# Optimization experiments

Hardware: AMD Instinct MI355X
Metric: run time of the kernel (lower is better)

The kernel has to match this reference:

```python
import jax, jax.numpy as jnp
import numpy as np

O, T = 100000, 400000
DIN = HID = DOUT = 128


def setup_inputs() -> dict:
    key = jax.random.key(0)
    ks = jax.random.split(key, 12)
    s = lambda fan_in: 1.0 / np.sqrt(fan_in)
    inp = {
        "obj_vecs": jax.random.normal(ks[0], (O, DIN), jnp.float32),
        "pred_vecs": jax.random.normal(ks[1], (T, DIN), jnp.float32),
        "edges": jax.random.randint(ks[2], (T, 2), 0, O, jnp.int64 if jax.config.read("jax_enable_x64") else jnp.int32),
        # net1: Linear(3*Din -> H), ReLU, Linear(H -> 2H + Dout)
        "W1a": jax.random.uniform(ks[3], (3 * DIN, HID), jnp.float32, -s(3 * DIN), s(3 * DIN)),
        "b1a": jax.random.uniform(ks[4], (HID,), jnp.float32, -s(3 * DIN), s(3 * DIN)),
        "W1b": jax.random.uniform(ks[5], (HID, 2 * HID + DOUT), jnp.float32, -s(HID), s(HID)),
        "b1b": jax.random.uniform(ks[6], (2 * HID + DOUT,), jnp.float32, -s(HID), s(HID)),
        # net2: Linear(H -> H), ReLU, Linear(H -> Dout)
        "W2a": jax.random.uniform(ks[7], (HID, HID), jnp.float32, -s(HID), s(HID)),
        "b2a": jax.random.uniform(ks[8], (HID,), jnp.float32, -s(HID), s(HID)),
        "W2b": jax.random.uniform(ks[9], (HID, DOUT), jnp.float32, -s(HID), s(HID)),
        "b2b": jax.random.uniform(ks[10], (DOUT,), jnp.float32, -s(HID), s(HID)),
    }
    return inp


def reference(obj_vecs, pred_vecs, edges, W1a, b1a, W1b, b1b, W2a, b2a, W2b, b2b):
    s_idx = edges[:, 0]
    o_idx = edges[:, 1]
    # 1. Triple formation: [h_s || r || h_o]  -> (T, 3*Din)
    t = jnp.concatenate([obj_vecs[s_idx], pred_vecs, obj_vecs[o_idx]], axis=1)
    # 2. net1 MLP
    h = jax.nn.relu(t @ W1a + b1a)
    new_t = h @ W1b + b1b  # (T, 2H + Dout)
    new_s = new_t[:, :HID]
    new_p = new_t[:, HID:HID + DOUT]
    new_o = new_t[:, HID + DOUT:]
    # 3. Scatter-add messages to nodes
    pooled = jax.ops.segment_sum(new_s, s_idx, num_segments=O)
    pooled = pooled + jax.ops.segment_sum(new_o, o_idx, num_segments=O)
    # 4. Average pooling by neighbor count (clamped to >= 1)
    ones = jnp.ones((T,), pooled.dtype)
    counts = jax.ops.segment_sum(ones, s_idx, num_segments=O)
    counts = counts + jax.ops.segment_sum(ones, o_idx, num_segments=O)
    pooled = pooled / jnp.maximum(counts, 1.0)[:, None]
    # 5. net2 node update
    new_obj = jax.nn.relu(pooled @ W2a + b2a) @ W2b + b2b
    return new_obj, new_p
```

## Files before the change

### kernel.cpp

```cpp
#include <hip/hip_runtime.h>
#include <hip/hip_bf16.h>
#include <stdint.h>

#define O_N 100000
#define T_N 400000
#define NCH1 1563
#define NCH3 391
#define NCHW 25000

typedef __attribute__((ext_vector_type(8))) short short8;
typedef __attribute__((ext_vector_type(4))) unsigned short us4;
typedef __attribute__((ext_vector_type(4))) float f32x4;
typedef __attribute__((ext_vector_type(16))) float f32x16;
typedef unsigned short ushort_t;

__device__ __forceinline__ unsigned short f2bf(float x) {
    union { float f; unsigned u; } v; v.f = x;
    unsigned u = v.u;
    unsigned rounded = u + 0x7FFF + ((u >> 16) & 1);
    return (unsigned short)(rounded >> 16);
}

__device__ __forceinline__ short8 pack8(f32x4 a, f32x4 b) {
    short8 t;
    t[0] = (short)f2bf(a[0]); t[1] = (short)f2bf(a[1]);
    t[2] = (short)f2bf(a[2]); t[3] = (short)f2bf(a[3]);
    t[4] = (short)f2bf(b[0]); t[5] = (short)f2bf(b[1]);
    t[6] = (short)f2bf(b[2]); t[7] = (short)f2bf(b[3]);
    return t;
}

__global__ void pack_b32(const float* __restrict__ W, ushort_t* __restrict__ out,
                         int Ksteps, int NT, int ldw, int col0) {
    int idx = blockIdx.x * 256 + threadIdx.x;
    int total = Ksteps * NT * 512;
    if (idx >= total) return;
    int j = idx & 7;
    int lane = (idx >> 3) & 63;
    int t2 = idx >> 9;
    int nt = t2 % NT;
    int ks = t2 / NT;
    int k = ks * 16 + ((lane >> 5) << 3) + j;
    int n = col0 + (nt << 5) + (lane & 31);
    out[idx] = f2bf(W[(size_t)k * ldw + n]);
}

__global__ void pack_b(const float* __restrict__ W, unsigned short* __restrict__ out,
                       int K, int Ntiles, int ldw, int col0) {
    int idx = blockIdx.x * 256 + threadIdx.x;
    int total = K * Ntiles * 16;
    if (idx >= total) return;
    int j = idx & 7;
    int lane = (idx >> 3) & 63;
    int t2 = idx >> 9;
    int ntile = t2 % Ntiles;
    int kstep = t2 / Ntiles;
    int k = kstep * 32 + ((lane >> 4) << 3) + j;
    int n = (ntile << 4) + (lane & 15);
    out[idx] = f2bf(W[(size_t)k * ldw + col0 + n]);
}

__global__ void counts_k(const int* __restrict__ edges, float* __restrict__ counts) {
    int idx = blockIdx.x * 256 + threadIdx.x;
    if (idx >= T_N) return;
    int2 e = ((const int2*)edges)[idx];
    atomicAdd(&counts[e.x], 1.0f);
    atomicAdd(&counts[e.y], 1.0f);
}

__global__ __launch_bounds__(1024, 4) void gemm1_k(
    const float* __restrict__ obj_vecs, const float* __restrict__ pred_vecs,
    const int* __restrict__ edges,
    const ushort_t* __restrict__ W1a_p, const float* __restrict__ b1a,
    ushort_t* __restrict__ hbuf)
{
    __shared__ __align__(16) ushort_t Wl[49152];
    __shared__ __align__(16) ushort_t hx[16][1088];
    const int tid = threadIdx.x;
    const int l = tid & 63;
    const int w = tid >> 6;
    const int r16 = l & 15;
    const int kq = l >> 4;

    {
        const short8* s = reinterpret_cast<const short8*>(W1a_p);
        short8* d = reinterpret_cast<short8*>(Wl);
        #pragma unroll
        for (int i = 0; i < 6; ++i) d[i * 1024 + tid] = s[i * 1024 + tid];
    }
    __syncthreads();

    float bias[8];
    #pragma unroll
    for (int nt = 0; nt < 8; ++nt) bias[nt] = b1a[nt * 16 + r16];

    ushort_t* hw = hx[w];
    const int2* e2 = (const int2*)edges;
    const int stride = gridDim.x * 16;

    for (int ch = blockIdx.x * 16 + w; ch < NCHW; ch += stride) {
        int tri = ch * 16 + r16;
        int2 e = e2[tri];
        const float* ps = obj_vecs  + (size_t)e.x * 128;
        const float* pp = pred_vecs + (size_t)tri * 128;
        const float* po = obj_vecs  + (size_t)e.y * 128;

        f32x4 acc[8];
        #pragma unroll
        for (int nt = 0; nt < 8; ++nt) acc[nt] = (f32x4){0.f, 0.f, 0.f, 0.f};

        {
            short8 af[4];
            #pragma unroll
            for (int ks = 0; ks < 4; ++ks) {
                f32x4 v0 = *reinterpret_cast<const f32x4*>(ps + ks * 32 + kq * 8);
                f32x4 v1 = *reinterpret_cast<const f32x4*>(ps + ks * 32 + kq * 8 + 4);
                af[ks] = pack8(v0, v1);
            }
            #pragma unroll
            for (int ks = 0; ks < 4; ++ks)
                #pragma unroll
                for (int nt = 0; nt < 8; ++nt) {
                    short8 b = *reinterpret_cast<const short8*>(&Wl[((ks * 8 + nt) * 64 + l) * 8]);
                    acc[nt] = __builtin_amdgcn_mfma_f32_16x16x32_bf16(af[ks], b, acc[nt], 0, 0, 0);
                }
        }
        {
            short8 af[4];
            #pragma unroll
            for (int ks = 0; ks < 4; ++ks) {
                f32x4 v0 = *reinterpret_cast<const f32x4*>(pp + ks * 32 + kq * 8);
                f32x4 v1 = *reinterpret_cast<const f32x4*>(pp + ks * 32 + kq * 8 + 4);
                af[ks] = pack8(v0, v1);
            }
            #pragma unroll
            for (int ks = 0; ks < 4; ++ks)
                #pragma unroll
                for (int nt = 0; nt < 8; ++nt) {
                    short8 b = *reinterpret_cast<const short8*>(&Wl[(((ks + 4) * 8 + nt) * 64 + l) * 8]);
                    acc[nt] = __builtin_amdgcn_mfma_f32_16x16x32_bf16(af[ks], b, acc[nt], 0, 0, 0);
                }
        }
        {
            short8 af[4];
            #pragma unroll
            for (int ks = 0; ks < 4; ++ks) {
                f32x4 v0 = *reinterpret_cast<const f32x4*>(po + ks * 32 + kq * 8);
                f32x4 v1 = *reinterpret_cast<const f32x4*>(po + ks * 32 + kq * 8 + 4);
                af[ks] = pack8(v0, v1);
            }
            #pragma unroll
            for (int ks = 0; ks < 4; ++ks)
                #pragma unroll
                for (int nt = 0; nt < 8; ++nt) {
                    short8 b = *reinterpret_cast<const short8*>(&Wl[(((ks + 8) * 8 + nt) * 64 + l) * 8]);
                    acc[nt] = __builtin_amdgcn_mfma_f32_16x16x32_bf16(af[ks], b, acc[nt], 0, 0, 0);
                }
        }

        #pragma unroll
        for (int p = 0; p < 2; ++p) {
            #pragma unroll
            for (int nt2 = 0; nt2 < 4; ++nt2) {
                int nt = p * 4 + nt2;
                #pragma unroll
                for (int j = 0; j < 4; ++j) {
                    int row = kq * 4 + j;
                    float hv = fmaxf(acc[nt][j] + bias[nt], 0.0f);
                    hw[row * 68 + nt2 * 16 + r16] = f2bf(hv);
                }
            }
            asm volatile("s_waitcnt lgkmcnt(0)" ::: "memory");
            #pragma unroll
            for (int it = 0; it < 2; ++it) {
                short8 hv = *reinterpret_cast<const short8*>(&hw[(l >> 2) * 68 + (l & 3) * 16 + it * 8]);
                *reinterpret_cast<short8*>(
                    &hbuf[(size_t)(ch * 16 + (l >> 2)) * 128 + p * 64 + (l & 3) * 16 + it * 8]) = hv;
            }
            asm volatile("s_waitcnt lgkmcnt(0)" ::: "memory");
        }
    }
}

__global__ __launch_bounds__(512, 2) void gemm2_k(
    const ushort_t* __restrict__ hbuf, const int* __restrict__ edges,
    const ushort_t* __restrict__ W1b_p, const float* __restrict__ b1b,
    ushort_t* __restrict__ pooled_bf, float* __restrict__ new_p)
{
    __shared__ __align__(16) ushort_t Wl[49152];
    const int tid = threadIdx.x;
    const int l = tid & 63;
    const int w = tid >> 6;
    const int q = l >> 5;
    const int r32 = l & 31;

    {
        const short8* s = reinterpret_cast<const short8*>(W1b_p);
        short8* d = reinterpret_cast<short8*>(Wl);
        #pragma unroll
        for (int i = 0; i < 12; ++i) d[i * 512 + tid] = s[i * 512 + tid];
    }
    __syncthreads();

    float bias[12];
    #pragma unroll
    for (int nt = 0; nt < 12; ++nt) bias[nt] = b1b[(nt << 5) + r32];

    for (int c = blockIdx.x; c < NCH1; c += gridDim.x) {
        int trow = c * 256 + w * 32 + r32;
        int tr = trow < T_N ? trow : T_N - 1;

        short8 af[8];
        #pragma unroll
        for (int ks = 0; ks < 8; ++ks)
            af[ks] = *reinterpret_cast<const short8*>(&hbuf[(size_t)tr * 128 + (ks << 4) + (q << 3)]);

        #pragma unroll
        for (int g = 0; g < 3; ++g) {
            f32x16 acc[4] = {};
            #pragma unroll
            for (int ks = 0; ks < 8; ++ks) {
                #pragma unroll
                for (int nt2 = 0; nt2 < 4; ++nt2) {
                    short8 bf = *reinterpret_cast<const short8*>(&Wl[((ks * 12 + (g << 2) + nt2) * 64 + l) * 8]);
                    acc[nt2] = __builtin_amdgcn_mfma_f32_32x32x16_bf16(af[ks], bf, acc[nt2], 0, 0, 0);
                }
            }
            if (g == 1) {
                #pragma unroll
                for (int nt2 = 0; nt2 < 4; ++nt2) {
                    #pragma unroll
                    for (int r = 0; r < 16; ++r) {
                        int rl = (r & 3) + ((r >> 2) << 3) + (q << 2);
                        int trow2 = c * 256 + w * 32 + rl;
                        if (trow2 < T_N)
                            new_p[(size_t)trow2 * 128 + (nt2 << 5) + r32] = acc[nt2][r] + bias[4 + nt2];
                    }
                }
            } else {
                #pragma unroll
                for (int r = 0; r < 16; ++r) {
                    int rl = (r & 3) + ((r >> 2) << 3) + (q << 2);
                    int trow2 = c * 256 + w * 32 + rl;
                    bool v2 = trow2 < T_N;
                    int t2 = v2 ? trow2 : T_N - 1;
                    int2 e2 = ((const int2*)edges)[t2];
                    int seg = (g == 0) ? e2.x : e2.y;
                    ushort_t* pb = pooled_bf + (size_t)seg * 128;
                    #pragma unroll
                    for (int nt2 = 0; nt2 < 4; ++nt2) {
                        float val = acc[nt2][r] + bias[(g << 2) + nt2];
                        float other = __shfl_xor(val, 1, 64);
                        if (v2 && !(r32 & 1)) {
                            unsigned dat = (unsigned)f2bf(val) | ((unsigned)f2bf(other) << 16);
                            uint64_t addr = (uint64_t)(uintptr_t)(pb + (nt2 << 5) + r32);
                            asm volatile("global_atomic_pk_add_bf16 %0, %1, off"
                                         :: "v"(addr), "v"(dat) : "memory");
                        }
                    }
                }
            }
        }
    }
}

__global__ __launch_bounds__(512, 2) void objects_k32(
    const ushort_t* __restrict__ pooled_bf, const float* __restrict__ counts,
    const ushort_t* __restrict__ W2a_p, const float* __restrict__ b2a,
    const ushort_t* __restrict__ W2b_p, const float* __restrict__ b2b,
    float* __restrict__ outp)
{
    __shared__ __align__(16) ushort_t Wa[16384];
    __shared__ __align__(16) ushort_t Wb[16384];
    __shared__ __align__(16) ushort_t hx[8][4096];
    const int tid = threadIdx.x;
    const int l = tid & 63;
    const int w = tid >> 6;
    const int q = l >> 5;
    const int r32 = l & 31;

    {
        const short8* sa = reinterpret_cast<const short8*>(W2a_p);
        const short8* sb = reinterpret_cast<const short8*>(W2b_p);
        short8* da = reinterpret_cast<short8*>(Wa);
        short8* db = reinterpret_cast<short8*>(Wb);
        #pragma unroll
        for (int i = 0; i < 4; ++i) { da[i * 512 + tid] = sa[i * 512 + tid]; db[i * 512 + tid] = sb[i * 512 + tid]; }
    }
    __syncthreads();

    float ba[4], bb[4];
    #pragma unroll
    for (int nt = 0; nt < 4; ++nt) { ba[nt] = b2a[(nt << 5) + r32]; bb[nt] = b2b[(nt << 5) + r32]; }

    for (int c = blockIdx.x; c < NCH3; c += gridDim.x) {
        int row = c * 256 + w * 32 + r32;
        int rr = row < O_N ? row : O_N - 1;
        float inv = 1.0f / fmaxf(counts[rr], 1.0f);

        short8 af[8];
        #pragma unroll
        for (int ks = 0; ks < 8; ++ks) {
            short8 raw = *reinterpret_cast<const short8*>(&pooled_bf[(size_t)rr * 128 + (ks << 4) + (q << 3)]);
            short8 a;
            #pragma unroll
            for (int j = 0; j < 8; ++j) {
                union { float f; unsigned u; } t;
                t.u = ((unsigned)(unsigned short)raw[j]) << 16;
                a[j] = (short)f2bf(t.f * inv);
            }
            af[ks] = a;
        }

        f32x16 acc[4] = {};
        #pragma unroll
        for (int ks = 0; ks < 8; ++ks) {
            #pragma unroll
            for (int nt = 0; nt < 4; ++nt) {
                short8 bf = *reinterpret_cast<const short8*>(&Wa[(((ks << 2) + nt) * 64 + l) * 8]);
                acc[nt] = __builtin_amdgcn_mfma_f32_32x32x16_bf16(af[ks], bf, acc[nt], 0, 0, 0);
            }
        }

        char* hxw = (char*)&hx[w][0];
        #pragma unroll
        for (int nt = 0; nt < 4; ++nt) {
            #pragma unroll
            for (int r = 0; r < 16; ++r) {
                int rl = (r & 3) + ((r >> 2) << 3) + (q << 2);
                float hv = fmaxf(acc[nt][r] + ba[nt], 0.0f);
                int off = rl * 256 + (((nt << 5) + r32) << 1);
                off ^= (rl & 15) << 4;
                *(ushort_t*)(hxw + off) = f2bf(hv);
            }
        }
        __syncthreads();

        short8 af2[8];
        #pragma unroll
        for (int ks = 0; ks < 8; ++ks) {
            int off = r32 * 256 + (ks << 5) + (q << 4);
            off ^= (r32 & 15) << 4;
            af2[ks] = *reinterpret_cast<const short8*>(hxw + off);
        }

        f32x16 acc2[4] = {};
        #pragma unroll
        for (int ks = 0; ks < 8; ++ks) {
            #pragma unroll
            for (int nt = 0; nt < 4; ++nt) {
                short8 bf = *reinterpret_cast<const short8*>(&Wb[(((ks << 2) + nt) * 64 + l) * 8]);
                acc2[nt] = __builtin_amdgcn_mfma_f32_32x32x16_bf16(af2[ks], bf, acc2[nt], 0, 0, 0);
            }
        }

        #pragma unroll
        for (int nt = 0; nt < 4; ++nt) {
            #pragma unroll
            for (int r = 0; r < 16; ++r) {
                int rl = (r & 3) + ((r >> 2) << 3) + (q << 2);
                int row2 = c * 256 + w * 32 + rl;
                if (row2 < O_N) outp[(size_t)row2 * 128 + (nt << 5) + r32] = acc2[nt][r] + bb[nt];
            }
        }
        __syncthreads();
    }
}

__device__ __forceinline__ void stage_w(const unsigned short* __restrict__ src,
                                        unsigned short* __restrict__ dst, int tid) {
    const short8* s = reinterpret_cast<const short8*>(src);
    short8* d = reinterpret_cast<short8*>(dst);
    d[tid] = s[tid];
    d[tid + 256] = s[tid + 256];
}

__global__ __launch_bounds__(256, 2) void triples_kernel(
    const float* __restrict__ obj_vecs, const float* __restrict__ pred_vecs,
    const int* __restrict__ edges,
    const unsigned short* __restrict__ W1a_p, const float* __restrict__ b1a,
    const unsigned short* __restrict__ W1b_p, const float* __restrict__ b1b,
    float* __restrict__ pooled, float* __restrict__ new_p, float* __restrict__ counts)
{
    __shared__ __align__(16) unsigned short Apack[24576];
    __shared__ __align__(16) unsigned short Wbuf[2][4096];
    __shared__ int sseg[64], oseg[64];
    const int tid = threadIdx.x;
    const int lane = tid & 63;
    const int w = tid >> 6;
    const int t0 = blockIdx.x * 64;
    if (tid < 64) {
        int s = edges[2 * (t0 + tid)];
        int o = edges[2 * (t0 + tid) + 1];
        sseg[tid] = s; oseg[tid] = o;
        atomicAdd(&counts[s], 1.0f);
        atomicAdd(&counts[o], 1.0f);
    }
    __syncthreads();
    for (int it = 0; it < 24; ++it) {
        int idx = it * 256 + tid;
        int r = idx / 96;
        int c = (idx % 96) * 4;
        const float* srcp;
        if (c < 128)      srcp = obj_vecs  + (size_t)sseg[r] * 128 + c;
        else if (c < 256) srcp = pred_vecs + (size_t)(t0 + r) * 128 + (c - 128);
        else              srcp = obj_vecs  + (size_t)oseg[r] * 128 + (c - 256);
        f32x4 v = *reinterpret_cast<const f32x4*>(srcp);
        int off = (((r >> 4) * 12 + (c >> 5)) << 9)
                + (((r & 15) | (((c & 31) >> 3) << 4)) << 3) + (c & 7);
        Apack[off + 0] = f2bf(v[0]); Apack[off + 1] = f2bf(v[1]);
        Apack[off + 2] = f2bf(v[2]); Apack[off + 3] = f2bf(v[3]);
    }
    stage_w(W1a_p, Wbuf[0], tid);
    __syncthreads();
    f32x4 acc[8];
    #pragma unroll
    for (int n = 0; n < 8; ++n) acc[n] = (f32x4){0.f, 0.f, 0.f, 0.f};
    for (int kk = 0; kk < 12; ++kk) {
        if (kk < 11) stage_w(W1a_p + (kk + 1) * 4096, Wbuf[(kk + 1) & 1], tid);
        short8 a = *reinterpret_cast<const short8*>(&Apack[((w * 12 + kk) << 9) + (lane << 3)]);
        const unsigned short* wb = Wbuf[kk & 1];
        #pragma unroll
        for (int n = 0; n < 8; ++n) {
            short8 b = *reinterpret_cast<const short8*>(&wb[((n << 6) + lane) << 3]);
            acc[n] = __builtin_amdgcn_mfma_f32_16x16x32_bf16(a, b, acc[n], 0, 0, 0);
        }
        __syncthreads();
    }
    #pragma unroll
    for (int n = 0; n < 8; ++n) {
        int col = (n << 4) + (lane & 15);
        float bias = b1a[col];
        int base = ((w * 4 + (col >> 5)) << 9) + (col & 7);
        int chi = ((col & 31) >> 3) << 4;
        #pragma unroll
        for (int jj = 0; jj < 4; ++jj) {
            int rloc = ((lane >> 4) << 2) + jj;
            float hv = acc[n][jj] + bias;
            hv = hv > 0.f ? hv : 0.f;
            Apack[base + ((rloc | chi) << 3)] = f2bf(hv);
        }
    }
    for (int g = 0; g < 3; ++g) {
        const unsigned short* Wsrc = W1b_p + g * 16384;
        stage_w(Wsrc, Wbuf[0], tid);
        __syncthreads();
        f32x4 acc2[8];
        #pragma unroll
        for (int n = 0; n < 8; ++n) acc2[n] = (f32x4){0.f, 0.f, 0.f, 0.f};
        for (int kk = 0; kk < 4; ++kk) {
            if (kk < 3) stage_w(Wsrc + (kk + 1) * 4096, Wbuf[(kk + 1) & 1], tid);
            short8 a = *reinterpret_cast<const short8*>(&Apack[((w * 4 + kk) << 9) + (lane << 3)]);
            const unsigned short* wb = Wbuf[kk & 1];
            #pragma unroll
            for (int n = 0; n < 8; ++n) {
                short8 b = *reinterpret_cast<const short8*>(&wb[((n << 6) + lane) << 3]);
                acc2[n] = __builtin_amdgcn_mfma_f32_16x16x32_bf16(a, b, acc2[n], 0, 0, 0);
            }
            __syncthreads();
        }
        #pragma unroll
        for (int n = 0; n < 8; ++n) {
            int col = (n << 4) + (lane & 15);
            float bias = b1b[g * 128 + col];
            #pragma unroll
            for (int jj = 0; jj < 4; ++jj) {
                int rloc = (w << 4) + ((lane >> 4) << 2) + jj;
                float val = acc2[n][jj] + bias;
                if (g == 1) {
                    new_p[(size_t)(t0 + rloc) * 128 + col] = val;
                } else {
                    int seg = (g == 0) ? sseg[rloc] : oseg[rloc];
                    atomicAdd(&pooled[(size_t)seg * 128 + col], val);
                }
            }
        }
    }
}

__global__ __launch_bounds__(256, 2) void objects_kernel(
    const float* __restrict__ counts,
    const unsigned short* __restrict__ W2a_p, const float* __restrict__ b2a,
    const unsigned short* __restrict__ W2b_p, const float* __restrict__ b2b,
    float* __restrict__ inout)
{
    __shared__ __align__(16) unsigned short Apack[8192];
    __shared__ __align__(16) unsigned short Hpack[8192];
    __shared__ __align__(16) unsigned short Wbuf[2][4096];
    const int tid = threadIdx.x;
    const int lane = tid & 63;
    const int w = tid >> 6;
    const int r0 = blockIdx.x * 64;
    for (int it = 0; it < 8; ++it) {
        int idx = it * 256 + tid;
        int r = idx >> 5;
        int c = (idx & 31) << 2;
        int row = r0 + r;
        float vals[4] = {0.f, 0.f, 0.f, 0.f};
        if (row < O_N) {
            f32x4 v = *reinterpret_cast<const f32x4*>(&inout[(size_t)row * 128 + c]);
            float inv = 1.0f / fmaxf(counts[row], 1.0f);
            vals[0] = v[0] * inv; vals[1] = v[1] * inv;
            vals[2] = v[2] * inv; vals[3] = v[3] * inv;
        }
        int off = (((r >> 4) * 4 + (c >> 5)) << 9)
                + (((r & 15) | (((c & 31) >> 3) << 4)) << 3) + (c & 7);
        Apack[off + 0] = f2bf(vals[0]); Apack[off + 1] = f2bf(vals[1]);
        Apack[off + 2] = f2bf(vals[2]); Apack[off + 3] = f2bf(vals[3]);
    }
    stage_w(W2a_p, Wbuf[0], tid);
    __syncthreads();
    f32x4 acc[8];
    #pragma unroll
    for (int n = 0; n < 8; ++n) acc[n] = (f32x4){0.f, 0.f, 0.f, 0.f};
    for (int kk = 0; kk < 4; ++kk) {
        if (kk < 3) stage_w(W2a_p + (kk + 1) * 4096, Wbuf[(kk + 1) & 1], tid);
        short8 a = *reinterpret_cast<const short8*>(&Apack[((w * 4 + kk) << 9) + (lane << 3)]);
        const unsigned short* wb = Wbuf[kk & 1];
        #pragma unroll
        for (int n = 0; n < 8; ++n) {
            short8 b = *reinterpret_cast<const short8*>(&wb[((n << 6) + lane) << 3]);
            acc[n] = __builtin_amdgcn_mfma_f32_16x16x32_bf16(a, b, acc[n], 0, 0, 0);
        }
        __syncthreads();
    }
    #pragma unroll
    for (int n = 0; n < 8; ++n) {
        int col = (n << 4) + (lane & 15);
        float bias = b2a[col];
        int base = ((w * 4 + (col >> 5)) << 9) + (col & 7);
        int chi = ((col & 31) >> 3) << 4;
        #pragma unroll
        for (int jj = 0; jj < 4; ++jj) {
            int rloc = ((lane >> 4) << 2) + jj;
            float hv = acc[n][jj] + bias;
            hv = hv > 0.f ? hv : 0.f;
            Hpack[base + ((rloc | chi) << 3)] = f2bf(hv);
        }
    }
    stage_w(W2b_p, Wbuf[0], tid);
    __syncthreads();
    f32x4 acc2[8];
    #pragma unroll
    for (int n = 0; n < 8; ++n) acc2[n] = (f32x4){0.f, 0.f, 0.f, 0.f};
    for (int kk = 0; kk < 4; ++kk) {
        if (kk < 3) stage_w(W2b_p + (kk + 1) * 4096, Wbuf[(kk + 1) & 1], tid);
        short8 a = *reinterpret_cast<const short8*>(&Hpack[((w * 4 + kk) << 9) + (lane << 3)]);
        const unsigned short* wb = Wbuf[kk & 1];
        #pragma unroll
        for (int n = 0; n < 8; ++n) {
            short8 b = *reinterpret_cast<const short8*>(&wb[((n << 6) + lane) << 3]);
            acc2[n] = __builtin_amdgcn_mfma_f32_16x16x32_bf16(a, b, acc2[n], 0, 0, 0);
        }
        __syncthreads();
    }
    #pragma unroll
    for (int n = 0; n < 8; ++n) {
        int col = (n << 4) + (lane & 15);
        float bias = b2b[col];
        #pragma unroll
        for (int jj = 0; jj < 4; ++jj) {
            int rloc = (w << 4) + ((lane >> 4) << 2) + jj;
            int row = r0 + rloc;
            if (row < O_N) inout[(size_t)row * 128 + col] = acc2[n][jj] + bias;
        }
    }
}

extern "C" void kernel_launch(void* const* d_in, const int* in_sizes, int n_in,
                              void* d_out, int out_size, void* d_ws, size_t ws_size,
                              hipStream_t stream)
{
    const float* obj   = (const float*)d_in[0];
    const float* pred  = (const float*)d_in[1];
    const int*   edges = (const int*)d_in[2];
    const float* W1a = (const float*)d_in[3];
    const float* b1a = (const float*)d_in[4];
    const float* W1b = (const float*)d_in[5];
    const float* b1b = (const float*)d_in[6];
    const float* W2a = (const float*)d_in[7];
    const float* b2a = (const float*)d_in[8];
    const float* W2b = (const float*)d_in[9];
    const float* b2b = (const float*)d_in[10];

    float* out    = (float*)d_out;
    float* new_p  = out + (size_t)O_N * 128;

    uintptr_t wsbase = (uintptr_t)d_ws;
    float* counts = (float*)wsbase;
    uintptr_t p = (wsbase + (size_t)O_N * 4 + 255) & ~(uintptr_t)255;
    ushort_t* pooled_bf = (ushort_t*)p;  p += (size_t)O_N * 128 * 2;
    ushort_t* W1a_p = (ushort_t*)p;  p += (size_t)49152 * 2;
    ushort_t* W1b_p = (ushort_t*)p;  p += (size_t)49152 * 2;
    ushort_t* W2a_p = (ushort_t*)p;  p += (size_t)16384 * 2;
    ushort_t* W2b_p = (ushort_t*)p;  p += (size_t)16384 * 2;
    ushort_t* hbuf  = (ushort_t*)p;  p += (size_t)T_N * 128 * 2;
    size_t need = p - wsbase;

    hipMemsetAsync(counts, 0, (size_t)O_N * sizeof(float), stream);

    if (ws_size >= need) {
        hipMemsetAsync(pooled_bf, 0, (size_t)O_N * 128 * 2, stream);

        pack_b<<<192, 256, 0, stream>>>(W1a, W1a_p, 384, 8, 128, 0);
        pack_b32<<<192, 256, 0, stream>>>(W1b, W1b_p, 8, 12, 384, 0);
        pack_b32<<<64, 256, 0, stream>>>(W2a, W2a_p, 8, 4, 128, 0);
        pack_b32<<<64, 256, 0, stream>>>(W2b, W2b_p, 8, 4, 128, 0);
        counts_k<<<(T_N + 255) / 256, 256, 0, stream>>>(edges, counts);

        gemm1_k<<<256, 1024, 0, stream>>>(obj, pred, edges, W1a_p, b1a, hbuf);
        gemm2_k<<<256, 512, 0, stream>>>(hbuf, edges, W1b_p, b1b, pooled_bf, new_p);
        objects_k32<<<391, 512, 0, stream>>>(pooled_bf, counts, W2a_p, b2a, W2b_p, b2b, out);
    } else {
        float* pooled = out;
        hipMemsetAsync(pooled, 0, (size_t)O_N * 128 * sizeof(float), stream);

        pack_b<<<192, 256, 0, stream>>>(W1a, W1a_p, 384, 8, 128, 0);
        pack_b<<<64, 256, 0, stream>>>(W1b, W1b_p,         128, 8, 384, 0);
        pack_b<<<64, 256, 0, stream>>>(W1b, W1b_p + 16384, 128, 8, 384, 128);
        pack_b<<<64, 256, 0, stream>>>(W1b, W1b_p + 32768, 128, 8, 384, 256);
        pack_b<<<64, 256, 0, stream>>>(W2a, W2a_p, 128, 8, 128, 0);
        pack_b<<<64, 256, 0, stream>>>(W2b, W2b_p, 128, 8, 128, 0);

        triples_kernel<<<T_N / 64, 256, 0, stream>>>(obj, pred, edges,
                                                     W1a_p, b1a, W1b_p, b1b,
                                                     pooled, new_p, counts);
        objects_kernel<<<(O_N + 63) / 64, 256, 0, stream>>>(counts, W2a_p, b2a, W2b_p, b2b, out);
    }
}
```

Measured before the change: 460.9 us.

## Scatter hidden activations before W1b and apply subject/object projections per node

Uses the linearity of the second net1 layer. The per-triple hidden vector h is scatter-added into per-node subject and object sums (Hs/Ho), and the W1b subject and object column blocks are applied once per node afterwards. Bias is added back scaled by the separate subject and object counts. This cuts gemm2 from three 128-column output groups per triple to only the new_p group, and moves mean normalisation into a new pooled_k node-level GEMM. The cost is an extra kernel and buffers aliased into the output region, while bf16 atomic accumulation now applies to h instead of to the outputs.

```diff
diff --git a/kernel.cpp b/kernel.cpp
--- a/kernel.cpp
+++ b/kernel.cpp
@@ -60,12 +60,27 @@
     out[idx] = f2bf(W[(size_t)k * ldw + col0 + n]);
 }
 
-__global__ void counts_k(const int* __restrict__ edges, float* __restrict__ counts) {
+__global__ void pack_bso(const float* __restrict__ W1b, ushort_t* __restrict__ out) {
+    int idx = blockIdx.x * 256 + threadIdx.x;
+    if (idx >= 32768) return;
+    int j = idx & 7;
+    int lane = (idx >> 3) & 63;
+    int t2 = idx >> 9;
+    int nt = t2 & 3;
+    int ks = t2 >> 2;
+    int k = ks * 16 + ((lane >> 5) << 3) + j;
+    int n = (nt << 5) + (lane & 31);
+    float v = (k < 128) ? W1b[(size_t)k * 384 + n] : W1b[(size_t)(k - 128) * 384 + 256 + n];
+    out[idx] = f2bf(v);
+}
+
+__global__ void counts_k(const int* __restrict__ edges,
+                         float* __restrict__ cs, float* __restrict__ co) {
     int idx = blockIdx.x * 256 + threadIdx.x;
     if (idx >= T_N) return;
     int2 e = ((const int2*)edges)[idx];
-    atomicAdd(&counts[e.x], 1.0f);
-    atomicAdd(&counts[e.y], 1.0f);
+    atomicAdd(&cs[e.x], 1.0f);
+    atomicAdd(&co[e.y], 1.0f);
 }
 
 __global__ __launch_bounds__(1024, 4) void gemm1_k(
@@ -182,90 +197,151 @@
     }
 }
 
-__global__ __launch_bounds__(512, 2) void gemm2_k(
+__global__ __launch_bounds__(512, 4) void gemm2_k(
     const ushort_t* __restrict__ hbuf, const int* __restrict__ edges,
     const ushort_t* __restrict__ W1b_p, const float* __restrict__ b1b,
-    ushort_t* __restrict__ pooled_bf, float* __restrict__ new_p)
+    ushort_t* __restrict__ Hs, ushort_t* __restrict__ Ho,
+    float* __restrict__ new_p)
 {
-    __shared__ __align__(16) ushort_t Wl[49152];
+    __shared__ __align__(16) ushort_t Wl[16384];
     const int tid = threadIdx.x;
     const int l = tid & 63;
     const int w = tid >> 6;
     const int q = l >> 5;
     const int r32 = l & 31;
 
-    {
-        const short8* s = reinterpret_cast<const short8*>(W1b_p);
-        short8* d = reinterpret_cast<short8*>(Wl);
-        #pragma unroll
-        for (int i = 0; i < 12; ++i) d[i * 512 + tid] = s[i * 512 + tid];
+    #pragma unroll
+    for (int i = 0; i < 4; ++i) {
+        int idx = i * 512 + tid;
+        int blk = idx >> 6;
+        int li = idx & 63;
+        reinterpret_cast<short8*>(Wl)[idx] =
+            *reinterpret_cast<const short8*>(&W1b_p[(((blk >> 2) * 12 + 4 + (blk & 3)) * 64 + li) * 8]);
     }
     __syncthreads();
 
-    float bias[12];
-    #pragma unroll
-    for (int nt = 0; nt < 12; ++nt) bias[nt] = b1b[(nt << 5) + r32];
+    float bias[4];
+    #pragma unroll
+    for (int nt = 0; nt < 4; ++nt) bias[nt] = b1b[128 + (nt << 5) + r32];
 
     for (int c = blockIdx.x; c < NCH1; c += gridDim.x) {
         int trow = c * 256 + w * 32 + r32;
-        int tr = trow < T_N ? trow : T_N - 1;
+        bool valid = trow < T_N;
+        int tr = valid ? trow : T_N - 1;
+        int2 e = ((const int2*)edges)[tr];
 
         short8 af[8];
         #pragma unroll
         for (int ks = 0; ks < 8; ++ks)
             af[ks] = *reinterpret_cast<const short8*>(&hbuf[(size_t)tr * 128 + (ks << 4) + (q << 3)]);
 
-        #pragma unroll
-        for (int g = 0; g < 3; ++g) {
-            f32x16 acc[4] = {};
+        if (valid) {
+            ushort_t* hs = Hs + (size_t)e.x * 128;
+            ushort_t* ho = Ho + (size_t)e.y * 128;
             #pragma unroll
             for (int ks = 0; ks < 8; ++ks) {
                 #pragma unroll
-                for (int nt2 = 0; nt2 < 4; ++nt2) {
-                    short8 bf = *reinterpret_cast<const short8*>(&Wl[((ks * 12 + (g << 2) + nt2) * 64 + l) * 8]);
-                    acc[nt2] = __builtin_amdgcn_mfma_f32_32x32x16_bf16(af[ks], bf, acc[nt2], 0, 0, 0);
+                for (int j = 0; j < 4; ++j) {
+                    unsigned dat = (unsigned)(unsigned short)af[ks][2 * j]
+                                 | ((unsigned)(unsigned short)af[ks][2 * j + 1] << 16);
+                    int coff = (ks << 4) + (q << 3) + 2 * j;
+                    asm volatile("global_atomic_pk_add_bf16 %0, %1, off"
+                                 :: "v"((uint64_t)(uintptr_t)(hs + coff)), "v"(dat) : "memory");
+                    asm volatile("global_atomic_pk_add_bf16 %0, %1, off"
+                                 :: "v"((uint64_t)(uintptr_t)(ho + coff)), "v"(dat) : "memory");
                 }
             }
-            if (g == 1) {
+        }
+
+        f32x16 acc[4] = {};
+        #pragma unroll
+        for (int ks = 0; ks < 8; ++ks) {
+            #pragma unroll
+            for (int nt2 = 0; nt2 < 4; ++nt2) {
+                short8 bf = *reinterpret_cast<const short8*>(&Wl[(((ks << 2) + nt2) * 64 + l) * 8]);
+                acc[nt2] = __builtin_amdgcn_mfma_f32_32x32x16_bf16(af[ks], bf, acc[nt2], 0, 0, 0);
+            }
+        }
+        #pragma unroll
+        for (int nt2 = 0; nt2 < 4; ++nt2) {
+            #pragma unroll
+            for (int r = 0; r < 16; ++r) {
+                int rl = (r & 3) + ((r >> 2) << 3) + (q << 2);
+                int trow2 = c * 256 + w * 32 + rl;
+                if (trow2 < T_N)
+                    new_p[(size_t)trow2 * 128 + (nt2 << 5) + r32] = acc[nt2][r] + bias[nt2];
+            }
+        }
+    }
+}
+
+__global__ __launch_bounds__(512, 4) void pooled_k(
+    const ushort_t* __restrict__ Hs, const ushort_t* __restrict__ Ho,
+    const float* __restrict__ cs, const float* __restrict__ co,
+    const ushort_t* __restrict__ Wso_p, const float* __restrict__ b1b,
+    ushort_t* __restrict__ pooled_bf)
+{
+    __shared__ __align__(16) ushort_t Wl[32768];
+    const int tid = threadIdx.x;
+    const int l = tid & 63;
+    const int w = tid >> 6;
+    const int q = l >> 5;
+    const int r32 = l & 31;
+
+    #pragma unroll
+    for (int i = 0; i < 8; ++i)
+        reinterpret_cast<short8*>(Wl)[i * 512 + tid] =
+            reinterpret_cast<const short8*>(Wso_p)[i * 512 + tid];
+    __syncthreads();
+
+    float bs[4], bo[4];
+    #pragma unroll
+    for (int nt = 0; nt < 4; ++nt) {
+        bs[nt] = b1b[(nt << 5) + r32];
+        bo[nt] = b1b[256 + (nt << 5) + r32];
+    }
+
+    for (int c = blockIdx.x; c < NCH3; c += gridDim.x) {
+        int row = c * 256 + w * 32 + r32;
+        int rr = row < O_N ? row : O_N - 1;
+
+        short8 af[16];
+        #pragma unroll
+        for (int ks = 0; ks < 8; ++ks)
+            af[ks] = *reinterpret_cast<const short8*>(&Hs[(size_t)rr * 128 + (ks << 4) + (q << 3)]);
+        #pragma unroll
+        for (int ks = 0; ks < 8; ++ks)
+            af[8 + ks] = *reinterpret_cast<const short8*>(&Ho[(size_t)rr * 128 + (ks << 4) + (q << 3)]);
+
+        f32x16 acc[4] = {};
+        #pragma unroll
+        for (int ks = 0; ks < 16; ++ks) {
+            #pragma unroll
+            for (int nt = 0; nt < 4; ++nt) {
+                short8 bf = *reinterpret_cast<const short8*>(&Wl[(((ks << 2) + nt) * 64 + l) * 8]);
+                acc[nt] = __builtin_amdgcn_mfma_f32_32x32x16_bf16(af[ks], bf, acc[nt], 0, 0, 0);
+            }
+        }
+
+        #pragma unroll
+        for (int r = 0; r < 16; ++r) {
+            int rl = (r & 3) + ((r >> 2) << 3) + (q << 2);
+            int row2 = c * 256 + w * 32 + rl;
+            if (row2 < O_N) {
+                float csv = cs[row2], cov = co[row2];
+                float inv = 1.0f / fmaxf(csv + cov, 1.0f);
                 #pragma unroll
-                for (int nt2 = 0; nt2 < 4; ++nt2) {
-                    #pragma unroll
-                    for (int r = 0; r < 16; ++r) {
-                        int rl = (r & 3) + ((r >> 2) << 3) + (q << 2);
-                        int trow2 = c * 256 + w * 32 + rl;
-                        if (trow2 < T_N)
-                            new_p[(size_t)trow2 * 128 + (nt2 << 5) + r32] = acc[nt2][r] + bias[4 + nt2];
-                    }
+                for (int nt = 0; nt < 4; ++nt) {
+                    float val = (acc[nt][r] + csv * bs[nt] + cov * bo[nt]) * inv;
+                    pooled_bf[(size_t)row2 * 128 + (nt << 5) + r32] = f2bf(val);
                 }
-            } else {
-                #pragma unroll
-                for (int r = 0; r < 16; ++r) {
-                    int rl = (r & 3) + ((r >> 2) << 3) + (q << 2);
-                    int trow2 = c * 256 + w * 32 + rl;
-                    bool v2 = trow2 < T_N;
-                    int t2 = v2 ? trow2 : T_N - 1;
-                    int2 e2 = ((const int2*)edges)[t2];
-                    int seg = (g == 0) ? e2.x : e2.y;
-                    ushort_t* pb = pooled_bf + (size_t)seg * 128;
-                    #pragma unroll
-                    for (int nt2 = 0; nt2 < 4; ++nt2) {
-                        float val = acc[nt2][r] + bias[(g << 2) + nt2];
-                        float other = __shfl_xor(val, 1, 64);
-                        if (v2 && !(r32 & 1)) {
-                            unsigned dat = (unsigned)f2bf(val) | ((unsigned)f2bf(other) << 16);
-                            uint64_t addr = (uint64_t)(uintptr_t)(pb + (nt2 << 5) + r32);
-                            asm volatile("global_atomic_pk_add_bf16 %0, %1, off"
-                                         :: "v"(addr), "v"(dat) : "memory");
-                        }
-                    }
-                }
-            }
-        }
-    }
-}
-
-__global__ __launch_bounds__(512, 2) void objects_k32(
-    const ushort_t* __restrict__ pooled_bf, const float* __restrict__ counts,
+            }
+        }
+    }
+}
+
+__global__ __launch_bounds__(512, 2) void objects_nd(
+    const ushort_t* __restrict__ pooled_bf,
     const ushort_t* __restrict__ W2a_p, const float* __restrict__ b2a,
     const ushort_t* __restrict__ W2b_p, const float* __restrict__ b2b,
     float* __restrict__ outp)
@@ -296,21 +372,11 @@
     for (int c = blockIdx.x; c < NCH3; c += gridDim.x) {
         int row = c * 256 + w * 32 + r32;
         int rr = row < O_N ? row : O_N - 1;
-        float inv = 1.0f / fmaxf(counts[rr], 1.0f);
 
         short8 af[8];
         #pragma unroll
-        for (int ks = 0; ks < 8; ++ks) {
-            short8 raw = *reinterpret_cast<const short8*>(&pooled_bf[(size_t)rr * 128 + (ks << 4) + (q << 3)]);
-            short8 a;
-            #pragma unroll
-            for (int j = 0; j < 8; ++j) {
-                union { float f; unsigned u; } t;
-                t.u = ((unsigned)(unsigned short)raw[j]) << 16;
-                a[j] = (short)f2bf(t.f * inv);
-            }
-            af[ks] = a;
-        }
+        for (int ks = 0; ks < 8; ++ks)
+            af[ks] = *reinterpret_cast<const short8*>(&pooled_bf[(size_t)rr * 128 + (ks << 4) + (q << 3)]);
 
         f32x16 acc[4] = {};
         #pragma unroll
@@ -586,33 +652,41 @@
     float* out    = (float*)d_out;
     float* new_p  = out + (size_t)O_N * 128;
 
+    ushort_t* Hs = (ushort_t*)d_out;
+    ushort_t* Ho = Hs + (size_t)O_N * 128;
+
     uintptr_t wsbase = (uintptr_t)d_ws;
     float* counts = (float*)wsbase;
-    uintptr_t p = (wsbase + (size_t)O_N * 4 + 255) & ~(uintptr_t)255;
+    float* cs = counts + O_N;
+    float* co = cs + O_N;
+    uintptr_t p = ((uintptr_t)(co + O_N) + 255) & ~(uintptr_t)255;
     ushort_t* pooled_bf = (ushort_t*)p;  p += (size_t)O_N * 128 * 2;
     ushort_t* W1a_p = (ushort_t*)p;  p += (size_t)49152 * 2;
     ushort_t* W1b_p = (ushort_t*)p;  p += (size_t)49152 * 2;
     ushort_t* W2a_p = (ushort_t*)p;  p += (size_t)16384 * 2;
     ushort_t* W2b_p = (ushort_t*)p;  p += (size_t)16384 * 2;
+    ushort_t* Wso_p = (ushort_t*)p;  p += (size_t)32768 * 2;
     ushort_t* hbuf  = (ushort_t*)p;  p += (size_t)T_N * 128 * 2;
     size_t need = p - wsbase;
 
-    hipMemsetAsync(counts, 0, (size_t)O_N * sizeof(float), stream);
-
     if (ws_size >= need) {
-        hipMemsetAsync(pooled_bf, 0, (size_t)O_N * 128 * 2, stream);
+        hipMemsetAsync(Hs, 0, (size_t)O_N * 128 * 2 * sizeof(ushort_t), stream);
+        hipMemsetAsync(cs, 0, (size_t)O_N * 2 * sizeof(float), stream);
 
         pack_b<<<192, 256, 0, stream>>>(W1a, W1a_p, 384, 8, 128, 0);
         pack_b32<<<192, 256, 0, stream>>>(W1b, W1b_p, 8, 12, 384, 0);
         pack_b32<<<64, 256, 0, stream>>>(W2a, W2a_p, 8, 4, 128, 0);
         pack_b32<<<64, 256, 0, stream>>>(W2b, W2b_p, 8, 4, 128, 0);
-        counts_k<<<(T_N + 255) / 256, 256, 0, stream>>>(edges, counts);
+        pack_bso<<<128, 256, 0, stream>>>(W1b, Wso_p);
+        counts_k<<<(T_N + 255) / 256, 256, 0, stream>>>(edges, cs, co);
 
         gemm1_k<<<256, 1024, 0, stream>>>(obj, pred, edges, W1a_p, b1a, hbuf);
-        gemm2_k<<<256, 512, 0, stream>>>(hbuf, edges, W1b_p, b1b, pooled_bf, new_p);
-        objects_k32<<<391, 512, 0, stream>>>(pooled_bf, counts, W2a_p, b2a, W2b_p, b2b, out);
+        gemm2_k<<<1024, 512, 0, stream>>>(hbuf, edges, W1b_p, b1b, Hs, Ho, new_p);
+        pooled_k<<<391, 512, 0, stream>>>(Hs, Ho, cs, co, Wso_p, b1b, pooled_bf);
+        objects_nd<<<391, 512, 0, stream>>>(pooled_bf, W2a_p, b2a, W2b_p, b2b, out);
     } else {
         float* pooled = out;
+        hipMemsetAsync(counts, 0, (size_t)O_N * sizeof(float), stream);
         hipMemsetAsync(pooled, 0, (size_t)O_N * 128 * sizeof(float), stream);
 
         pack_b<<<192, 256, 0, stream>>>(W1a, W1a_p, 384, 8, 128, 0);
```

Result: slower. 1.655 ms (+259.1%).

## Split second GEMM into scatter and predicate kernels with higher occupancy

Applied to the files above, without the earlier changes.

The fused second-layer GEMM kernel is split into two kernels. One computes the subject/object slices and scatters them with packed bf16 atomics, the other computes the predicate slice and writes new_p. Each kernel stages a smaller LDS weight slice (64KB or 32KB instead of 96KB), raises launch bounds to 4 blocks per CU, and launches 1024 blocks instead of 256. In exchange, the hbuf activations are read twice from global memory and there is an extra kernel launch.

```diff
diff --git a/kernel.cpp b/kernel.cpp
--- a/kernel.cpp
+++ b/kernel.cpp
@@ -182,29 +182,31 @@
     }
 }
 
-__global__ __launch_bounds__(512, 2) void gemm2_k(
-    const ushort_t* __restrict__ hbuf, const int* __restrict__ edges,
+__global__ __launch_bounds__(512, 4) void gemm2_p(
+    const ushort_t* __restrict__ hbuf,
     const ushort_t* __restrict__ W1b_p, const float* __restrict__ b1b,
-    ushort_t* __restrict__ pooled_bf, float* __restrict__ new_p)
+    float* __restrict__ new_p)
 {
-    __shared__ __align__(16) ushort_t Wl[49152];
+    __shared__ __align__(16) ushort_t Wl[16384];
     const int tid = threadIdx.x;
     const int l = tid & 63;
     const int w = tid >> 6;
     const int q = l >> 5;
     const int r32 = l & 31;
 
-    {
-        const short8* s = reinterpret_cast<const short8*>(W1b_p);
-        short8* d = reinterpret_cast<short8*>(Wl);
-        #pragma unroll
-        for (int i = 0; i < 12; ++i) d[i * 512 + tid] = s[i * 512 + tid];
-    }
-    __syncthreads();
-
-    float bias[12];
-    #pragma unroll
-    for (int nt = 0; nt < 12; ++nt) bias[nt] = b1b[(nt << 5) + r32];
+    #pragma unroll
+    for (int i = 0; i < 4; ++i) {
+        int idx = i * 512 + tid;
+        int blk = idx >> 6;
+        int li = idx & 63;
+        reinterpret_cast<short8*>(Wl)[idx] =
+            *reinterpret_cast<const short8*>(&W1b_p[(((blk >> 2) * 12 + 4 + (blk & 3)) * 64 + li) * 8]);
+    }
+    __syncthreads();
+
+    float bias[4];
+    #pragma unroll
+    for (int nt = 0; nt < 4; ++nt) bias[nt] = b1b[128 + (nt << 5) + r32];
 
     for (int c = blockIdx.x; c < NCH1; c += gridDim.x) {
         int trow = c * 256 + w * 32 + r32;
@@ -215,48 +217,98 @@
         for (int ks = 0; ks < 8; ++ks)
             af[ks] = *reinterpret_cast<const short8*>(&hbuf[(size_t)tr * 128 + (ks << 4) + (q << 3)]);
 
-        #pragma unroll
-        for (int g = 0; g < 3; ++g) {
+        f32x16 acc[4] = {};
+        #pragma unroll
+        for (int ks = 0; ks < 8; ++ks) {
+            #pragma unroll
+            for (int nt2 = 0; nt2 < 4; ++nt2) {
+                short8 bf = *reinterpret_cast<const short8*>(&Wl[(((ks << 2) + nt2) * 64 + l) * 8]);
+                acc[nt2] = __builtin_amdgcn_mfma_f32_32x32x16_bf16(af[ks], bf, acc[nt2], 0, 0, 0);
+            }
+        }
+        #pragma unroll
+        for (int nt2 = 0; nt2 < 4; ++nt2) {
+            #pragma unroll
+            for (int r = 0; r < 16; ++r) {
+                int rl = (r & 3) + ((r >> 2) << 3) + (q << 2);
+                int trow2 = c * 256 + w * 32 + rl;
+                if (trow2 < T_N)
+                    new_p[(size_t)trow2 * 128 + (nt2 << 5) + r32] = acc[nt2][r] + bias[nt2];
+            }
+        }
+    }
+}
+
+__global__ __launch_bounds__(512, 4) void gemm2_so(
+    const ushort_t* __restrict__ hbuf, const int* __restrict__ edges,
+    const ushort_t* __restrict__ W1b_p, const float* __restrict__ b1b,
+    ushort_t* __restrict__ pooled_bf)
+{
+    __shared__ __align__(16) ushort_t Wl[32768];
+    const int tid = threadIdx.x;
+    const int l = tid & 63;
+    const int w = tid >> 6;
+    const int q = l >> 5;
+    const int r32 = l & 31;
+
+    #pragma unroll
+    for (int i = 0; i < 8; ++i) {
+        int idx = i * 512 + tid;
+        int blk = idx >> 6;
+        int li = idx & 63;
+        int ks = blk >> 3;
+        int gg = (blk >> 2) & 1;
+        int nt2 = blk & 3;
+        reinterpret_cast<short8*>(Wl)[idx] =
+            *reinterpret_cast<const short8*>(&W1b_p[((ks * 12 + (gg ? 8 : 0) + nt2) * 64 + li) * 8]);
+    }
+    __syncthreads();
+
+    float bs[4], bo[4];
+    #pragma unroll
+    for (int nt = 0; nt < 4; ++nt) {
+        bs[nt] = b1b[(nt << 5) + r32];
+        bo[nt] = b1b[256 + (nt << 5) + r32];
+    }
+
+    for (int c = blockIdx.x; c < NCH1; c += gridDim.x) {
+        int trow = c * 256 + w * 32 + r32;
+        int tr = trow < T_N ? trow : T_N - 1;
+
+        short8 af[8];
+        #pragma unroll
+        for (int ks = 0; ks < 8; ++ks)
+            af[ks] = *reinterpret_cast<const short8*>(&hbuf[(size_t)tr * 128 + (ks << 4) + (q << 3)]);
+
+        #pragma unroll
+        for (int gg = 0; gg < 2; ++gg) {
             f32x16 acc[4] = {};
             #pragma unroll
             for (int ks = 0; ks < 8; ++ks) {
                 #pragma unroll
                 for (int nt2 = 0; nt2 < 4; ++nt2) {
-                    short8 bf = *reinterpret_cast<const short8*>(&Wl[((ks * 12 + (g << 2) + nt2) * 64 + l) * 8]);
+                    short8 bf = *reinterpret_cast<const short8*>(&Wl[(((ks << 3) + (gg << 2) + nt2) * 64 + l) * 8]);
                     acc[nt2] = __builtin_amdgcn_mfma_f32_32x32x16_bf16(af[ks], bf, acc[nt2], 0, 0, 0);
                 }
             }
-            if (g == 1) {
+            #pragma unroll
+            for (int r = 0; r < 16; ++r) {
+                int rl = (r & 3) + ((r >> 2) << 3) + (q << 2);
+                int trow2 = c * 256 + w * 32 + rl;
+                bool v2 = trow2 < T_N;
+                int t2 = v2 ? trow2 : T_N - 1;
+                int2 e2 = ((const int2*)edges)[t2];
+                int seg = gg ? e2.y : e2.x;
+                ushort_t* pb = pooled_bf + (size_t)seg * 128;
                 #pragma unroll
                 for (int nt2 = 0; nt2 < 4; ++nt2) {
-                    #pragma unroll
-                    for (int r = 0; r < 16; ++r) {
-                        int rl = (r & 3) + ((r >> 2) << 3) + (q << 2);
-                        int trow2 = c * 256 + w * 32 + rl;
-                        if (trow2 < T_N)
-                            new_p[(size_t)trow2 * 128 + (nt2 << 5) + r32] = acc[nt2][r] + bias[4 + nt2];
-                    }
-                }
-            } else {
-                #pragma unroll
-                for (int r = 0; r < 16; ++r) {
-                    int rl = (r & 3) + ((r >> 2) << 3) + (q << 2);
-                    int trow2 = c * 256 + w * 32 + rl;
-                    bool v2 = trow2 < T_N;
-                    int t2 = v2 ? trow2 : T_N - 1;
-                    int2 e2 = ((const int2*)edges)[t2];
-                    int seg = (g == 0) ? e2.x : e2.y;
-                    ushort_t* pb = pooled_bf + (size_t)seg * 128;
-                    #pragma unroll
-                    for (int nt2 = 0; nt2 < 4; ++nt2) {
-                        float val = acc[nt2][r] + bias[(g << 2) + nt2];
-                        float other = __shfl_xor(val, 1, 64);
-                        if (v2 && !(r32 & 1)) {
-                            unsigned dat = (unsigned)f2bf(val) | ((unsigned)f2bf(other) << 16);
-                            uint64_t addr = (uint64_t)(uintptr_t)(pb + (nt2 << 5) + r32);
-                            asm volatile("global_atomic_pk_add_bf16 %0, %1, off"
-                                         :: "v"(addr), "v"(dat) : "memory");
-                        }
+                    float val = acc[nt2][r] + (gg ? bo[nt2] : bs[nt2]);
+                    float other = __shfl_xor(val, 1, 64);
+                    if (v2 && !(r32 & 1)) {
+                        unsigned dat = (unsigned)f2bf(val) | ((unsigned)f2bf(other) << 16);
+                        uint64_t addr = (uint64_t)(uintptr_t)(pb + (nt2 << 5) + r32);
+                        asm volatile("global_atomic_pk_add_bf16 %0, %1, off"
+                                     :: "v"(addr), "v"(dat) : "memory");
                     }
                 }
             }
@@ -609,7 +661,8 @@
         counts_k<<<(T_N + 255) / 256, 256, 0, stream>>>(edges, counts);
 
         gemm1_k<<<256, 1024, 0, stream>>>(obj, pred, edges, W1a_p, b1a, hbuf);
-        gemm2_k<<<256, 512, 0, stream>>>(hbuf, edges, W1b_p, b1b, pooled_bf, new_p);
+        gemm2_so<<<1024, 512, 0, stream>>>(hbuf, edges, W1b_p, b1b, pooled_bf);
+        gemm2_p<<<1024, 512, 0, stream>>>(hbuf, W1b_p, b1b, new_p);
         objects_k32<<<391, 512, 0, stream>>>(pooled_bf, counts, W2a_p, b2a, W2b_p, b2b, out);
     } else {
         float* pooled = out;
```

Result: slower. 574.8 us (+24.7%).
